# Optimization experiments

Hardware: AMD Instinct MI355X
Metric: run time of the kernel (lower is better)

Reference implementation:

```python
import jax, jax.numpy as jnp
import numpy as np

EMBED_DIM = 512
SMOOTH = 4.0        # args.lambda_softmax
LAMBDA_LSE = 6.0    # args.lambda_lse
LEAKY_SLOPE = 0.1
EPS = 1e-8


def setup_inputs() -> dict:
    key = jax.random.key(0)
    k1, k2, k3 = jax.random.split(key, 3)
    n_contract, n_region = 32, 256
    n_law, max_len = 32, 256
    contracts = jax.random.normal(k1, (n_contract, n_region, EMBED_DIM), jnp.float32)
    laws = jax.random.normal(k2, (n_law, max_len, EMBED_DIM), jnp.float32)
    law_lens = jax.random.randint(k3, (n_law,), 128, max_len + 1, jnp.int32)
    return {"contracts": contracts, "laws": laws, "law_lens": law_lens}


def reference(contracts, laws, law_lens):
    # contracts: [C, R, D], laws: [N, L, D], law_lens: [N]
    n_law, max_len, d = laws.shape
    # mask[n, l] = 1 if word l is within law n's true length
    mask = (jnp.arange(max_len)[None, :] < law_lens[:, None]).astype(contracts.dtype)

    # attn = law @ contract^T / sqrt(D): [N, C, L, R]
    attn = jnp.einsum('nld,crd->nclr', laws, contracts) / jnp.sqrt(jnp.float32(d))
    attn = jax.nn.leaky_relu(attn, LEAKY_SLOPE)
    # l2norm over region dim (per law-word row)
    attn = attn / (jnp.linalg.norm(attn, axis=-1, keepdims=True) + EPS)
    attn = jax.nn.softmax(attn, axis=-1) * SMOOTH
    # zero out contributions from padded law words (ragged lengths)
    attn = attn * mask[:, None, :, None]

    # weighted_law: [N, C, R, D]
    wlaw = jnp.einsum('nld,nclr->ncrd', laws, attn)

    # cosine similarity along D: [N, C, R]
    w12 = jnp.sum(contracts[None] * wlaw, axis=-1)
    w1 = jnp.linalg.norm(contracts, axis=-1)[None]          # [1, C, R]
    w2 = jnp.linalg.norm(wlaw, axis=-1)                      # [N, C, R]
    sim = w12 / jnp.maximum(w1 * w2, EPS)

    # LogSumExp aggregation over regions -> [N, C]
    row_sim = jnp.log(jnp.sum(jnp.exp(sim * LAMBDA_LSE), axis=-1)) / LAMBDA_LSE
    # concatenate per-law columns -> [C, N]
    return row_sim.T
```

## Files before the change

### kernel.cpp

```cpp
#include <hip/hip_runtime.h>
#include <hip/hip_bf16.h>

#define CN 32
#define RN 256
#define DN 512
#define NN 32
#define LN 256

#define STAGE_OFF 131072
#define SMEM_TOTAL 163840

typedef short v8s __attribute__((ext_vector_type(8)));
typedef float v4f __attribute__((ext_vector_type(4)));
typedef const __attribute__((address_space(1))) void* gas1_t;
typedef __attribute__((address_space(3))) void* las3_t;

__device__ __forceinline__ void gl2lds16(const void* g, void* l) {
  __builtin_amdgcn_global_load_lds((gas1_t)g, (las3_t)l, 16, 0, 0);
}

__device__ __forceinline__ unsigned short f2bf(float x) {
  unsigned int u = __float_as_uint(x);
  u = (u + 0x7fffu + ((u >> 16) & 1u)) >> 16;
  return (unsigned short)u;
}
__device__ __forceinline__ float bf2f(unsigned short h) {
  return __uint_as_float(((unsigned int)h) << 16);
}

__device__ __forceinline__ const v8s* stgFrag(const unsigned short* buf, int r,
                                              int quad) {
  return (const v8s*)(buf + r * 32 + ((quad ^ ((r >> 1) & 3)) << 3));
}

__device__ __forceinline__ int satIdx(int r, int col) {
  return (r << 8) | ((((col >> 3) ^ (r & 7)) << 3) | (col & 7));
}

__global__ __launch_bounds__(256) void prep_kernel(
    const float* __restrict__ con, const float* __restrict__ laws,
    unsigned short* __restrict__ lawsB, unsigned short* __restrict__ conB,
    float* __restrict__ cnorm) {
  const int bid = blockIdx.x;
  const int t = threadIdx.x;
  if (bid < 2048) {
    const int r = bid * 4 + (t >> 6);
    const int lane = t & 63;
    const float4* src = (const float4*)(con + r * DN + lane * 8);
    float4 x0 = src[0], x1 = src[1];
    unsigned short h[8];
    h[0] = f2bf(x0.x); h[1] = f2bf(x0.y); h[2] = f2bf(x0.z); h[3] = f2bf(x0.w);
    h[4] = f2bf(x1.x); h[5] = f2bf(x1.y); h[6] = f2bf(x1.z); h[7] = f2bf(x1.w);
    *(v8s*)(conB + r * DN + lane * 8) = *(v8s*)h;
    float s = x0.x * x0.x + x0.y * x0.y + x0.z * x0.z + x0.w * x0.w +
              x1.x * x1.x + x1.y * x1.y + x1.z * x1.z + x1.w * x1.w;
#pragma unroll
    for (int m = 1; m < 64; m <<= 1) s += __shfl_xor(s, m, 64);
    if (lane == 0) cnorm[r] = sqrtf(s);
  } else {
    const int off = (bid - 2048) * 2048 + t * 8;
    const float4* src = (const float4*)(laws + off);
    float4 x0 = src[0], x1 = src[1];
    unsigned short h[8];
    h[0] = f2bf(x0.x); h[1] = f2bf(x0.y); h[2] = f2bf(x0.z); h[3] = f2bf(x0.w);
    h[4] = f2bf(x1.x); h[5] = f2bf(x1.y); h[6] = f2bf(x1.z); h[7] = f2bf(x1.w);
    *(v8s*)(lawsB + off) = *(v8s*)h;
  }
}

__global__ __launch_bounds__(512) void gramm_kernel(
    const unsigned short* __restrict__ lawsB, unsigned short* __restrict__ G) {
  __shared__ unsigned short lawsAll[256 * 32];
  __shared__ unsigned short lawsSub[64 * 32];
  const int bx = blockIdx.x;
  const int n = bx >> 2;
  const int m0 = (bx & 3) << 6;
  const int t = threadIdx.x;
  const int lane = t & 63;
  const int w = t >> 6;
  const int quad = lane >> 4;
  const int l16 = lane & 15;
  const int sub = t & 3;
  const int rQ = t >> 2;
  const int subx = sub ^ ((rQ >> 1) & 3);
  const unsigned short* lawN = lawsB + n * (LN * DN);
  const int wr = (w & 1) << 5;
  const int wc = (w >> 1) << 6;

  v4f acc[2][4];
#pragma unroll
  for (int a = 0; a < 2; ++a)
#pragma unroll
    for (int b = 0; b < 4; ++b) acc[a][b] = (v4f){0.f, 0.f, 0.f, 0.f};

  for (int ch = 0; ch < 16; ++ch) {
    const int dk = ch << 5;
    __syncthreads();
#pragma unroll
    for (int i = 0; i < 2; ++i)
      gl2lds16(lawN + (i * 128 + rQ) * DN + dk + subx * 8,
               (char*)lawsAll + i * 8192 + t * 16);
    if (t < 256)
      gl2lds16(lawN + (m0 + rQ) * DN + dk + subx * 8, (char*)lawsSub + t * 16);
    __syncthreads();
    v8s af0 = *stgFrag(lawsSub, wr + l16, quad);
    v8s af1 = *stgFrag(lawsSub, wr + 16 + l16, quad);
#pragma unroll
    for (int rt = 0; rt < 4; ++rt) {
      v8s bf = *stgFrag(lawsAll, wc + rt * 16 + l16, quad);
      acc[0][rt] = __builtin_amdgcn_mfma_f32_16x16x32_bf16(af0, bf, acc[0][rt], 0, 0, 0);
      acc[1][rt] = __builtin_amdgcn_mfma_f32_16x16x32_bf16(af1, bf, acc[1][rt], 0, 0, 0);
    }
  }
  unsigned short* g = G + n * (LN * LN);
#pragma unroll
  for (int tl = 0; tl < 2; ++tl)
#pragma unroll
    for (int reg = 0; reg < 4; ++reg) {
      const int l = m0 + wr + tl * 16 + quad * 4 + reg;
#pragma unroll
      for (int rt = 0; rt < 4; ++rt)
        g[l * LN + wc + rt * 16 + l16] = f2bf(acc[tl][rt][reg]);
    }
}

__global__ __launch_bounds__(1024, 4) void main_kernel(
    const int* __restrict__ law_lens, const unsigned short* __restrict__ lawsB,
    const unsigned short* __restrict__ conB, const unsigned short* __restrict__ Gm,
    const float* __restrict__ cnorm, float* __restrict__ out) {
  extern __shared__ char smem[];
  unsigned short* sAt = (unsigned short*)smem;
  char* stage = smem + STAGE_OFF;

  const int bid = blockIdx.x;
  const int n = bid >> 5;
  const int c = bid & 31;
  const int t = threadIdx.x;
  const int lane = t & 63;
  const int w = t >> 6;
  const int quad = lane >> 4;
  const int l16 = lane & 15;
  const int sub = t & 3;
  const int rQ = t >> 2;
  const int subx = sub ^ ((rQ >> 1) & 3);
  const int len = law_lens[n];

  const unsigned short* lawN = lawsB + n * (LN * DN);
  const unsigned short* conC = conB + c * (RN * DN);
  const unsigned short* Gn = Gm + n * (LN * LN);

  float w12p[16];
#pragma unroll
  for (int i = 0; i < 16; ++i) w12p[i] = 0.f;

  {
    const unsigned short* a0p = lawN + (w * 16 + l16) * DN + quad * 8;

    v4f acc[16];
#pragma unroll
    for (int b = 0; b < 16; ++b) acc[b] = (v4f){0.f, 0.f, 0.f, 0.f};

    gl2lds16(conC + rQ * DN + subx * 8, stage + t * 16);

    for (int ch = 0; ch < 16; ++ch) {
      const int dk = ch << 5;
      __syncthreads();
      v8s af = *(const v8s*)(a0p + dk);
      __builtin_amdgcn_sched_barrier(0);
      if (ch < 15)
        gl2lds16(conC + rQ * DN + (dk + 32) + subx * 8,
                 stage + ((ch + 1) & 1) * 16384 + t * 16);
      __builtin_amdgcn_sched_barrier(0);
      const unsigned short* cs =
          (const unsigned short*)(stage + (ch & 1) * 16384);
#pragma unroll
      for (int rt = 0; rt < 16; ++rt) {
        v8s bf = *stgFrag(cs, rt * 16 + l16, quad);
        acc[rt] = __builtin_amdgcn_mfma_f32_16x16x32_bf16(af, bf, acc[rt], 0, 0, 0);
      }
    }
#pragma unroll
    for (int reg = 0; reg < 4; ++reg) {
      const int lg = w * 16 + quad * 4 + reg;
      float ss = 0.f;
#pragma unroll
      for (int rt = 0; rt < 16; ++rt) {
        const float v = acc[rt][reg] * 0.04419417382415922f;
        const float lv = v > 0.f ? v : 0.1f * v;
        ss += lv * lv;
      }
#pragma unroll
      for (int m = 1; m < 16; m <<= 1) ss += __shfl_xor(ss, m, 64);
      const float inv = 1.f / (sqrtf(ss) + 1e-8f);
      float den = 0.f;
#pragma unroll
      for (int rt = 0; rt < 16; ++rt) {
        const float v = acc[rt][reg] * 0.04419417382415922f;
        const float lv = v > 0.f ? v : 0.1f * v;
        den += __expf(lv * inv);
      }
#pragma unroll
      for (int m = 1; m < 16; m <<= 1) den += __shfl_xor(den, m, 64);
      const float sc = (lg < len) ? 4.f / den : 0.f;
#pragma unroll
      for (int rt = 0; rt < 16; ++rt) {
        const float v = acc[rt][reg] * 0.04419417382415922f;
        const float lv = v > 0.f ? v : 0.1f * v;
        const float a = __expf(lv * inv) * sc;
        w12p[rt] += a * v;
        sAt[satIdx(rt * 16 + l16, lg)] = f2bf(a);
      }
    }
  }

  __syncthreads();

  gl2lds16(Gn + rQ * LN + subx * 8, stage + t * 16);

#pragma unroll
  for (int rt = 0; rt < 16; ++rt) {
    w12p[rt] += __shfl_xor(w12p[rt], 16, 64);
    w12p[rt] += __shfl_xor(w12p[rt], 32, 64);
  }

  float nsv[4];
  {
    v4f acc[16];
#pragma unroll
    for (int b = 0; b < 16; ++b) acc[b] = (v4f){0.f, 0.f, 0.f, 0.f};

    for (int ch = 0; ch < 8; ++ch) {
      const int lk = ch << 5;
      __syncthreads();
      v8s af = *(const v8s*)(sAt + satIdx(w * 16 + l16, lk + quad * 8));
      __builtin_amdgcn_sched_barrier(0);
      if (ch < 7)
        gl2lds16(Gn + rQ * LN + (lk + 32) + subx * 8,
                 stage + ((ch + 1) & 1) * 16384 + t * 16);
      __builtin_amdgcn_sched_barrier(0);
      const unsigned short* gs =
          (const unsigned short*)(stage + (ch & 1) * 16384);
#pragma unroll
      for (int lt = 0; lt < 16; ++lt) {
        v8s bf = *stgFrag(gs, lt * 16 + l16, quad);
        acc[lt] = __builtin_amdgcn_mfma_f32_16x16x32_bf16(af, bf, acc[lt], 0, 0, 0);
      }
    }
#pragma unroll
    for (int reg = 0; reg < 4; ++reg) {
      const int r = w * 16 + quad * 4 + reg;
      float s = 0.f;
#pragma unroll
      for (int lt = 0; lt < 16; ++lt)
        s += acc[lt][reg] * bf2f(sAt[satIdx(r, lt * 16 + l16)]);
#pragma unroll
      for (int m = 1; m < 16; m <<= 1) s += __shfl_xor(s, m, 64);
      nsv[reg] = s;
    }
  }

  float* w12s = (float*)stage;
  float* nsqS = (float*)(stage + 16384);
  float* red = (float*)(stage + 17408);
  __syncthreads();
  if (l16 == 0) {
#pragma unroll
    for (int reg = 0; reg < 4; ++reg)
      nsqS[w * 16 + quad * 4 + reg] = nsv[reg];
  }
  if (lane < 16) {
#pragma unroll
    for (int rt = 0; rt < 16; ++rt) w12s[w * 256 + rt * 16 + lane] = w12p[rt];
  }
  __syncthreads();
  float p = 0.f;
  if (t < 256) {
    float w12 = 0.f;
#pragma unroll
    for (int i = 0; i < 16; ++i) w12 += w12s[i * 256 + t];
    const float w1 = cnorm[c * RN + t];
    const float w2 = sqrtf(fmaxf(nsqS[t], 0.f));
    const float sim = (w12 * 22.627416997969522f) / fmaxf(w1 * w2, 1e-8f);
    p = __expf(6.f * sim);
  }
#pragma unroll
  for (int m = 1; m < 64; m <<= 1) p += __shfl_xor(p, m, 64);
  if (t < 256 && lane == 0) red[w] = p;
  __syncthreads();
  if (t == 0) {
    out[c * NN + n] = logf(red[0] + red[1] + red[2] + red[3]) / 6.f;
  }
}

extern "C" void kernel_launch(void* const* d_in, const int* in_sizes, int n_in,
                              void* d_out, int out_size, void* d_ws, size_t ws_size,
                              hipStream_t stream) {
  (void)in_sizes; (void)n_in; (void)out_size;
  const float* contracts = (const float*)d_in[0];
  const float* laws = (const float*)d_in[1];
  const int* law_lens = (const int*)d_in[2];
  float* out = (float*)d_out;

  unsigned short* lawsB = (unsigned short*)d_ws;
  unsigned short* conB = lawsB + NN * LN * DN;
  unsigned short* G = conB + CN * RN * DN;
  float* cnorm = (float*)(G + NN * LN * LN);
  if (ws_size < (size_t)21004288) return;

  hipFuncSetAttribute((const void*)main_kernel,
                      hipFuncAttributeMaxDynamicSharedMemorySize, SMEM_TOTAL);

  prep_kernel<<<4096, 256, 0, stream>>>(contracts, laws, lawsB, conB, cnorm);
  gramm_kernel<<<128, 512, 0, stream>>>(lawsB, G);
  main_kernel<<<1024, 1024, SMEM_TOTAL, stream>>>(law_lens, lawsB, conB, G,
                                                  cnorm, out);
}
```

Measured before the change: 249.6 us.

## Retile main kernel GEMMs into 4x4 wave tiles with cross-wave row reductions

The main kernel's two MFMA phases switch from each wave owning 16 rows across all 256 columns to a 4x4 grid of 64x64 wave tiles. Each A fragment and B fragment is now reused across four MFMAs, which cuts LDS fragment reads per MFMA. The cost is that the row norm, softmax denominator, w12 and nsq reductions must be combined across waves through LDS, adding several barriers. The gram kernel is also retiled to 32-row blocks, doubling its grid and dropping the separate sub-slice load.

```diff
diff --git a/kernel.cpp b/kernel.cpp
--- a/kernel.cpp
+++ b/kernel.cpp
@@ -70,11 +70,10 @@
 
 __global__ __launch_bounds__(512) void gramm_kernel(
     const unsigned short* __restrict__ lawsB, unsigned short* __restrict__ G) {
-  __shared__ unsigned short lawsAll[256 * 32];
-  __shared__ unsigned short lawsSub[64 * 32];
+  __shared__ unsigned short slice[256 * 32];
   const int bx = blockIdx.x;
-  const int n = bx >> 2;
-  const int m0 = (bx & 3) << 6;
+  const int n = bx >> 3;
+  const int m0 = (bx & 7) << 5;
   const int t = threadIdx.x;
   const int lane = t & 63;
   const int w = t >> 6;
@@ -83,15 +82,13 @@
   const int sub = t & 3;
   const int rQ = t >> 2;
   const int subx = sub ^ ((rQ >> 1) & 3);
+  const int rg = w >> 2;
+  const int cg = w & 3;
   const unsigned short* lawN = lawsB + n * (LN * DN);
-  const int wr = (w & 1) << 5;
-  const int wc = (w >> 1) << 6;
-
-  v4f acc[2][4];
-#pragma unroll
-  for (int a = 0; a < 2; ++a)
-#pragma unroll
-    for (int b = 0; b < 4; ++b) acc[a][b] = (v4f){0.f, 0.f, 0.f, 0.f};
+
+  v4f acc[4];
+#pragma unroll
+  for (int b = 0; b < 4; ++b) acc[b] = (v4f){0.f, 0.f, 0.f, 0.f};
 
   for (int ch = 0; ch < 16; ++ch) {
     const int dk = ch << 5;
@@ -99,28 +96,22 @@
 #pragma unroll
     for (int i = 0; i < 2; ++i)
       gl2lds16(lawN + (i * 128 + rQ) * DN + dk + subx * 8,
-               (char*)lawsAll + i * 8192 + t * 16);
-    if (t < 256)
-      gl2lds16(lawN + (m0 + rQ) * DN + dk + subx * 8, (char*)lawsSub + t * 16);
+               (char*)slice + i * 8192 + t * 16);
     __syncthreads();
-    v8s af0 = *stgFrag(lawsSub, wr + l16, quad);
-    v8s af1 = *stgFrag(lawsSub, wr + 16 + l16, quad);
-#pragma unroll
-    for (int rt = 0; rt < 4; ++rt) {
-      v8s bf = *stgFrag(lawsAll, wc + rt * 16 + l16, quad);
-      acc[0][rt] = __builtin_amdgcn_mfma_f32_16x16x32_bf16(af0, bf, acc[0][rt], 0, 0, 0);
-      acc[1][rt] = __builtin_amdgcn_mfma_f32_16x16x32_bf16(af1, bf, acc[1][rt], 0, 0, 0);
+    v8s af = *stgFrag(slice, m0 + rg * 16 + l16, quad);
+#pragma unroll
+    for (int ct = 0; ct < 4; ++ct) {
+      v8s bf = *stgFrag(slice, cg * 64 + ct * 16 + l16, quad);
+      acc[ct] = __builtin_amdgcn_mfma_f32_16x16x32_bf16(af, bf, acc[ct], 0, 0, 0);
     }
   }
   unsigned short* g = G + n * (LN * LN);
 #pragma unroll
-  for (int tl = 0; tl < 2; ++tl)
-#pragma unroll
-    for (int reg = 0; reg < 4; ++reg) {
-      const int l = m0 + wr + tl * 16 + quad * 4 + reg;
-#pragma unroll
-      for (int rt = 0; rt < 4; ++rt)
-        g[l * LN + wc + rt * 16 + l16] = f2bf(acc[tl][rt][reg]);
+  for (int ct = 0; ct < 4; ++ct)
+#pragma unroll
+    for (int reg = 0; reg < 4; ++reg) {
+      const int l = m0 + rg * 16 + quad * 4 + reg;
+      g[l * LN + cg * 64 + ct * 16 + l16] = f2bf(acc[ct][reg]);
     }
 }
 
@@ -143,153 +134,199 @@
   const int sub = t & 3;
   const int rQ = t >> 2;
   const int subx = sub ^ ((rQ >> 1) & 3);
+  const int rg = w >> 2;
+  const int cg = w & 3;
+  const int rbase = rg << 6;
+  const int cbase = cg << 6;
   const int len = law_lens[n];
+  const float kInv = 0.04419417382415922f;
 
   const unsigned short* lawN = lawsB + n * (LN * DN);
   const unsigned short* conC = conB + c * (RN * DN);
   const unsigned short* Gn = Gm + n * (LN * LN);
 
-  float w12p[16];
-#pragma unroll
-  for (int i = 0; i < 16; ++i) w12p[i] = 0.f;
-
-  {
-    const unsigned short* a0p = lawN + (w * 16 + l16) * DN + quad * 8;
-
-    v4f acc[16];
-#pragma unroll
-    for (int b = 0; b < 16; ++b) acc[b] = (v4f){0.f, 0.f, 0.f, 0.f};
-
-    gl2lds16(conC + rQ * DN + subx * 8, stage + t * 16);
-
-    for (int ch = 0; ch < 16; ++ch) {
-      const int dk = ch << 5;
-      __syncthreads();
-      v8s af = *(const v8s*)(a0p + dk);
-      __builtin_amdgcn_sched_barrier(0);
-      if (ch < 15)
-        gl2lds16(conC + rQ * DN + (dk + 32) + subx * 8,
-                 stage + ((ch + 1) & 1) * 16384 + t * 16);
-      __builtin_amdgcn_sched_barrier(0);
-      const unsigned short* cs =
-          (const unsigned short*)(stage + (ch & 1) * 16384);
-#pragma unroll
-      for (int rt = 0; rt < 16; ++rt) {
-        v8s bf = *stgFrag(cs, rt * 16 + l16, quad);
-        acc[rt] = __builtin_amdgcn_mfma_f32_16x16x32_bf16(af, bf, acc[rt], 0, 0, 0);
+  float* ssP = (float*)stage;
+  float* denP = (float*)(stage + 4096);
+  float* w12P = (float*)(stage + 16384);
+  float* nsqP = (float*)stage;
+  float* red = (float*)(stage + 8192);
+
+  v4f acc[4][4];
+#pragma unroll
+  for (int a = 0; a < 4; ++a)
+#pragma unroll
+    for (int b = 0; b < 4; ++b) acc[a][b] = (v4f){0.f, 0.f, 0.f, 0.f};
+
+  gl2lds16(conC + rQ * DN + subx * 8, stage + t * 16);
+
+  for (int ch = 0; ch < 16; ++ch) {
+    const int dk = ch << 5;
+    __syncthreads();
+    v8s af[4];
+#pragma unroll
+    for (int rt = 0; rt < 4; ++rt)
+      af[rt] = *(const v8s*)(lawN + (rbase + rt * 16 + l16) * DN + dk + quad * 8);
+    __builtin_amdgcn_sched_barrier(0);
+    if (ch < 15)
+      gl2lds16(conC + rQ * DN + (dk + 32) + subx * 8,
+               stage + ((ch + 1) & 1) * 16384 + t * 16);
+    __builtin_amdgcn_sched_barrier(0);
+    const unsigned short* cs = (const unsigned short*)(stage + (ch & 1) * 16384);
+#pragma unroll
+    for (int ct = 0; ct < 4; ++ct) {
+      v8s bf = *stgFrag(cs, cbase + ct * 16 + l16, quad);
+#pragma unroll
+      for (int rt = 0; rt < 4; ++rt)
+        acc[rt][ct] = __builtin_amdgcn_mfma_f32_16x16x32_bf16(af[rt], bf, acc[rt][ct], 0, 0, 0);
+    }
+  }
+
+#pragma unroll
+  for (int rt = 0; rt < 4; ++rt)
+#pragma unroll
+    for (int reg = 0; reg < 4; ++reg) {
+      float ssp = 0.f;
+#pragma unroll
+      for (int ct = 0; ct < 4; ++ct) {
+        const float v = acc[rt][ct][reg] * kInv;
+        const float lv = v > 0.f ? v : 0.1f * v;
+        ssp += lv * lv;
       }
-    }
-#pragma unroll
-    for (int reg = 0; reg < 4; ++reg) {
-      const int lg = w * 16 + quad * 4 + reg;
-      float ss = 0.f;
-#pragma unroll
-      for (int rt = 0; rt < 16; ++rt) {
-        const float v = acc[rt][reg] * 0.04419417382415922f;
+#pragma unroll
+      for (int m = 1; m < 16; m <<= 1) ssp += __shfl_xor(ssp, m, 64);
+      if (l16 == 0)
+        ssP[(rbase + rt * 16 + quad * 4 + reg) * 4 + cg] = ssp;
+    }
+  __syncthreads();
+
+#pragma unroll
+  for (int rt = 0; rt < 4; ++rt)
+#pragma unroll
+    for (int reg = 0; reg < 4; ++reg) {
+      const int row = rbase + rt * 16 + quad * 4 + reg;
+      const float4 s4 = *(const float4*)&ssP[row * 4];
+      const float inv = 1.f / (sqrtf(s4.x + s4.y + s4.z + s4.w) + 1e-8f);
+      float dnp = 0.f;
+#pragma unroll
+      for (int ct = 0; ct < 4; ++ct) {
+        const float v = acc[rt][ct][reg] * kInv;
         const float lv = v > 0.f ? v : 0.1f * v;
-        ss += lv * lv;
+        dnp += __expf(lv * inv);
       }
 #pragma unroll
-      for (int m = 1; m < 16; m <<= 1) ss += __shfl_xor(ss, m, 64);
-      const float inv = 1.f / (sqrtf(ss) + 1e-8f);
-      float den = 0.f;
-#pragma unroll
-      for (int rt = 0; rt < 16; ++rt) {
-        const float v = acc[rt][reg] * 0.04419417382415922f;
+      for (int m = 1; m < 16; m <<= 1) dnp += __shfl_xor(dnp, m, 64);
+      if (l16 == 0) denP[row * 4 + cg] = dnp;
+    }
+  __syncthreads();
+
+  float w12c[4] = {0.f, 0.f, 0.f, 0.f};
+#pragma unroll
+  for (int rt = 0; rt < 4; ++rt) {
+    const int row0 = rbase + rt * 16 + quad * 4;
+    float invv[4], scv[4];
+#pragma unroll
+    for (int reg = 0; reg < 4; ++reg) {
+      const float4 s4 = *(const float4*)&ssP[(row0 + reg) * 4];
+      invv[reg] = 1.f / (sqrtf(s4.x + s4.y + s4.z + s4.w) + 1e-8f);
+      const float4 d4 = *(const float4*)&denP[(row0 + reg) * 4];
+      scv[reg] = (row0 + reg < len) ? 4.f / (d4.x + d4.y + d4.z + d4.w) : 0.f;
+    }
+#pragma unroll
+    for (int ct = 0; ct < 4; ++ct) {
+      unsigned int p0 = 0, p1 = 0;
+#pragma unroll
+      for (int reg = 0; reg < 4; ++reg) {
+        const float v = acc[rt][ct][reg] * kInv;
         const float lv = v > 0.f ? v : 0.1f * v;
-        den += __expf(lv * inv);
+        const float a = __expf(lv * invv[reg]) * scv[reg];
+        w12c[ct] += a * v;
+        const unsigned int h = f2bf(a);
+        if (reg == 0) p0 = h;
+        else if (reg == 1) p0 |= h << 16;
+        else if (reg == 2) p1 = h;
+        else p1 |= h << 16;
       }
-#pragma unroll
-      for (int m = 1; m < 16; m <<= 1) den += __shfl_xor(den, m, 64);
-      const float sc = (lg < len) ? 4.f / den : 0.f;
-#pragma unroll
-      for (int rt = 0; rt < 16; ++rt) {
-        const float v = acc[rt][reg] * 0.04419417382415922f;
-        const float lv = v > 0.f ? v : 0.1f * v;
-        const float a = __expf(lv * inv) * sc;
-        w12p[rt] += a * v;
-        sAt[satIdx(rt * 16 + l16, lg)] = f2bf(a);
-      }
-    }
-  }
-
-  __syncthreads();
+      uint2 pk; pk.x = p0; pk.y = p1;
+      *(uint2*)(sAt + satIdx(cbase + ct * 16 + l16, row0)) = pk;
+    }
+  }
+#pragma unroll
+  for (int ct = 0; ct < 4; ++ct) {
+    w12c[ct] += __shfl_xor(w12c[ct], 16, 64);
+    w12c[ct] += __shfl_xor(w12c[ct], 32, 64);
+  }
+  if (quad == 0) {
+#pragma unroll
+    for (int ct = 0; ct < 4; ++ct)
+      w12P[(cbase + ct * 16 + l16) * 4 + rg] = w12c[ct];
+  }
+  __syncthreads();
+
+  float w12f = 0.f;
+  if (t < 256) {
+    const float4 q = *(const float4*)&w12P[t * 4];
+    w12f = q.x + q.y + q.z + q.w;
+  }
 
   gl2lds16(Gn + rQ * LN + subx * 8, stage + t * 16);
 
-#pragma unroll
-  for (int rt = 0; rt < 16; ++rt) {
-    w12p[rt] += __shfl_xor(w12p[rt], 16, 64);
-    w12p[rt] += __shfl_xor(w12p[rt], 32, 64);
-  }
-
-  float nsv[4];
-  {
-    v4f acc[16];
-#pragma unroll
-    for (int b = 0; b < 16; ++b) acc[b] = (v4f){0.f, 0.f, 0.f, 0.f};
-
-    for (int ch = 0; ch < 8; ++ch) {
-      const int lk = ch << 5;
-      __syncthreads();
-      v8s af = *(const v8s*)(sAt + satIdx(w * 16 + l16, lk + quad * 8));
-      __builtin_amdgcn_sched_barrier(0);
-      if (ch < 7)
-        gl2lds16(Gn + rQ * LN + (lk + 32) + subx * 8,
-                 stage + ((ch + 1) & 1) * 16384 + t * 16);
-      __builtin_amdgcn_sched_barrier(0);
-      const unsigned short* gs =
-          (const unsigned short*)(stage + (ch & 1) * 16384);
-#pragma unroll
-      for (int lt = 0; lt < 16; ++lt) {
-        v8s bf = *stgFrag(gs, lt * 16 + l16, quad);
-        acc[lt] = __builtin_amdgcn_mfma_f32_16x16x32_bf16(af, bf, acc[lt], 0, 0, 0);
-      }
-    }
-#pragma unroll
-    for (int reg = 0; reg < 4; ++reg) {
-      const int r = w * 16 + quad * 4 + reg;
+  v4f accB[4][4];
+#pragma unroll
+  for (int a = 0; a < 4; ++a)
+#pragma unroll
+    for (int b = 0; b < 4; ++b) accB[a][b] = (v4f){0.f, 0.f, 0.f, 0.f};
+
+  for (int ch = 0; ch < 8; ++ch) {
+    const int lk = ch << 5;
+    __syncthreads();
+    v8s af[4];
+#pragma unroll
+    for (int rt = 0; rt < 4; ++rt)
+      af[rt] = *(const v8s*)(sAt + satIdx(rbase + rt * 16 + l16, lk + quad * 8));
+    __builtin_amdgcn_sched_barrier(0);
+    if (ch < 7)
+      gl2lds16(Gn + rQ * LN + (lk + 32) + subx * 8,
+               stage + ((ch + 1) & 1) * 16384 + t * 16);
+    __builtin_amdgcn_sched_barrier(0);
+    const unsigned short* gs = (const unsigned short*)(stage + (ch & 1) * 16384);
+#pragma unroll
+    for (int ct = 0; ct < 4; ++ct) {
+      v8s bf = *stgFrag(gs, cbase + ct * 16 + l16, quad);
+#pragma unroll
+      for (int rt = 0; rt < 4; ++rt)
+        accB[rt][ct] = __builtin_amdgcn_mfma_f32_16x16x32_bf16(af[rt], bf, accB[rt][ct], 0, 0, 0);
+    }
+  }
+
+#pragma unroll
+  for (int rt = 0; rt < 4; ++rt)
+#pragma unroll
+    for (int reg = 0; reg < 4; ++reg) {
+      const int row = rbase + rt * 16 + quad * 4 + reg;
       float s = 0.f;
 #pragma unroll
-      for (int lt = 0; lt < 16; ++lt)
-        s += acc[lt][reg] * bf2f(sAt[satIdx(r, lt * 16 + l16)]);
+      for (int ct = 0; ct < 4; ++ct)
+        s += accB[rt][ct][reg] * bf2f(sAt[satIdx(row, cbase + ct * 16 + l16)]);
 #pragma unroll
       for (int m = 1; m < 16; m <<= 1) s += __shfl_xor(s, m, 64);
-      nsv[reg] = s;
-    }
-  }
-
-  float* w12s = (float*)stage;
-  float* nsqS = (float*)(stage + 16384);
-  float* red = (float*)(stage + 17408);
-  __syncthreads();
-  if (l16 == 0) {
-#pragma unroll
-    for (int reg = 0; reg < 4; ++reg)
-      nsqS[w * 16 + quad * 4 + reg] = nsv[reg];
-  }
-  if (lane < 16) {
-#pragma unroll
-    for (int rt = 0; rt < 16; ++rt) w12s[w * 256 + rt * 16 + lane] = w12p[rt];
-  }
-  __syncthreads();
+      if (l16 == 0) nsqP[row * 4 + cg] = s;
+    }
+  __syncthreads();
+
   float p = 0.f;
   if (t < 256) {
-    float w12 = 0.f;
-#pragma unroll
-    for (int i = 0; i < 16; ++i) w12 += w12s[i * 256 + t];
+    const float4 q = *(const float4*)&nsqP[t * 4];
+    const float nsq = q.x + q.y + q.z + q.w;
     const float w1 = cnorm[c * RN + t];
-    const float w2 = sqrtf(fmaxf(nsqS[t], 0.f));
-    const float sim = (w12 * 22.627416997969522f) / fmaxf(w1 * w2, 1e-8f);
+    const float w2 = sqrtf(fmaxf(nsq, 0.f));
+    const float sim = (w12f * 22.627416997969522f) / fmaxf(w1 * w2, 1e-8f);
     p = __expf(6.f * sim);
   }
 #pragma unroll
   for (int m = 1; m < 64; m <<= 1) p += __shfl_xor(p, m, 64);
   if (t < 256 && lane == 0) red[w] = p;
   __syncthreads();
-  if (t == 0) {
-    out[c * NN + n] = logf(red[0] + red[1] + red[2] + red[3]) / 6.f;
-  }
+  if (t == 0) out[c * NN + n] = logf(red[0] + red[1] + red[2] + red[3]) / 6.f;
 }
 
 extern "C" void kernel_launch(void* const* d_in, const int* in_sizes, int n_in,
@@ -311,7 +348,7 @@
                       hipFuncAttributeMaxDynamicSharedMemorySize, SMEM_TOTAL);
 
   prep_kernel<<<4096, 256, 0, stream>>>(contracts, laws, lawsB, conB, cnorm);
-  gramm_kernel<<<128, 512, 0, stream>>>(lawsB, G);
+  gramm_kernel<<<256, 512, 0, stream>>>(lawsB, G);
   main_kernel<<<1024, 1024, SMEM_TOTAL, stream>>>(law_lens, lawsB, conB, G,
                                                   cnorm, out);
 }
```

New measurement: 440.0 us. 1.76x slower.
